# Kernel tuning notes

Measured on AMD Instinct MI355X. Metric: run time of the kernel, lower is better.

## Reference

```python
import jax, jax.numpy as jnp
jax.config.update("jax_enable_x64", True)
import numpy as np

B, S, D, H = 2, 1024, 1024, 16
DEPTH = D // H  # 64


def setup_inputs() -> dict:
    key = jax.random.key(0)
    ks = jax.random.split(key, 12)
    inp = {
        "q": jax.random.normal(ks[0], (B, S, D), jnp.float32),
        "k": jax.random.normal(ks[1], (B, S, D), jnp.float32),
        "v": jax.random.normal(ks[2], (B, S - 1, D), jnp.float32),
        "e": jnp.zeros((1,), jnp.float32),  # unused by the layer
        "mask": jax.random.randint(ks[3], (B, S - 1, S - 1), 0, 2, jnp.int32),
        "Wq": jax.random.normal(ks[4], (D, D), jnp.float32) * 0.02,
        "bq": jnp.zeros((D,), jnp.float32),
        "Wk": jax.random.normal(ks[5], (D, D), jnp.float32) * 0.02,
        "bk": jnp.zeros((D,), jnp.float32),
        "Wv": jax.random.normal(ks[6], (D, D), jnp.float32) * 0.02,
        "bv": jnp.zeros((D,), jnp.float32),
        "Wo": jax.random.normal(ks[7], (D, D), jnp.float32) * 0.02,
        "bo": jnp.zeros((D,), jnp.float32),
    }
    return inp


def _split_heads(x, b):
    # [b, s, D] -> [b, H, s, DEPTH]
    return x.reshape(b, -1, H, DEPTH).transpose(0, 2, 1, 3)


def reference(q, k, v, e, mask, Wq, bq, Wk, bk, Wv, bv, Wo, bo):
    b = q.shape[0]
    qh = _split_heads(q @ Wq + bq, b)  # [b,H,S,dh]
    kh = _split_heads(k @ Wk + bk, b)  # [b,H,S,dh]
    vh = _split_heads(v @ Wv + bv, b)  # [b,H,S-1,dh]
    # QK^T then asymmetric offset slice [1:, :-1]
    scores = jnp.einsum("bhqd,bhkd->bhqk", qh, kh)[:, :, 1:, :-1]  # [b,H,S-1,S-1]
    inv_sqrt_dk = 1.0 / jnp.sqrt(jnp.float32(DEPTH))
    nl_qk = jax.nn.relu(scores * inv_sqrt_dk).astype(jnp.float64)
    nl_qk = nl_qk + mask[:, None, :, :].astype(jnp.float64) * (-1e9)
    att_weights = jax.nn.softmax(nl_qk, axis=-1)  # fp64, [b,H,S-1,S-1]
    out = jnp.einsum("bhqk,bhkd->bhqd", att_weights, vh.astype(jnp.float64))
    out = out.transpose(0, 2, 1, 3).reshape(b, -1, H * DEPTH)  # [b,S-1,D]
    output = out.astype(jnp.float32) @ Wo + bo
    return (output, att_weights)
```

## Files before the change

kernel.cpp:

```cpp
#include <hip/hip_runtime.h>
#include <math.h>

#define HN 16
#define SEQ 1024
#define DMODEL 1024
#define DH 64
#define SM1 1023

typedef float  f32x4  __attribute__((ext_vector_type(4)));
typedef __bf16 bf16x8 __attribute__((ext_vector_type(8)));

#define GLD16(gsrc, ldst) \
    __builtin_amdgcn_global_load_lds((const __attribute__((address_space(1))) void*)(gsrc), \
                                     (__attribute__((address_space(3))) void*)(ldst), 16, 0, 0)

template<int MODE>
__global__ __launch_bounds__(256)
void gemm_mfma_kernel(const float* __restrict__ X, const float* __restrict__ W,
                      const float* __restrict__ bias, float* __restrict__ out32,
                      __bf16* __restrict__ outHi, __bf16* __restrict__ outLo,
                      int M, int rows)
{
    __shared__ __align__(16) __bf16 As[2][4096];
    __shared__ __align__(16) __bf16 Bs[2][4096];

    const int t  = threadIdx.x;
    const int w  = t >> 6, l = t & 63;
    const int lr = l & 15, ls = l >> 4;
    const int m0 = blockIdx.y * 64, n0 = blockIdx.x * 64;
    const int sr  = t >> 2;
    const int skq = t & 3;
    const bool arow_ok = (m0 + sr < M);

    f32x4 acc[4];
#pragma unroll
    for (int ct = 0; ct < 4; ++ct) acc[ct] = f32x4{0.f, 0.f, 0.f, 0.f};

    const int ar   = w * 16 + lr;
    const int a_hi = ar * 128 + (((2 * ls    ) ^ (ar & 7)) << 4);
    const int a_lo = ar * 128 + (((2 * ls + 1) ^ (ar & 7)) << 4);
    const int st_hi = sr * 128 + (((2 * skq    ) ^ (sr & 7)) << 4);
    const int st_lo = sr * 128 + (((2 * skq + 1) ^ (sr & 7)) << 4);

    float4 xv0, xv1;
    float  wv[8];

    auto LOADT = [&](int k0) {
        if (arow_ok) {
            xv0 = *(const float4*)&X[(size_t)(m0 + sr) * DMODEL + k0 + skq * 8];
            xv1 = *(const float4*)&X[(size_t)(m0 + sr) * DMODEL + k0 + skq * 8 + 4];
        } else {
            xv0 = float4{0.f, 0.f, 0.f, 0.f};
            xv1 = float4{0.f, 0.f, 0.f, 0.f};
        }
#pragma unroll
        for (int e = 0; e < 8; ++e)
            wv[e] = W[(size_t)(k0 + skq * 8 + e) * DMODEL + n0 + sr];
    };
    auto WRITET = [&](int buf) {
        float xa[8] = {xv0.x, xv0.y, xv0.z, xv0.w, xv1.x, xv1.y, xv1.z, xv1.w};
        bf16x8 ah8, al8, bh8, bl8;
#pragma unroll
        for (int e = 0; e < 8; ++e) {
            __bf16 hb = (__bf16)xa[e];
            ah8[e] = hb;
            al8[e] = (__bf16)(xa[e] - (float)hb);
            __bf16 wb = (__bf16)wv[e];
            bh8[e] = wb;
            bl8[e] = (__bf16)(wv[e] - (float)wb);
        }
        *(bf16x8*)((char*)As[buf] + st_hi) = ah8;
        *(bf16x8*)((char*)As[buf] + st_lo) = al8;
        *(bf16x8*)((char*)Bs[buf] + st_hi) = bh8;
        *(bf16x8*)((char*)Bs[buf] + st_lo) = bl8;
    };

    LOADT(0);
    WRITET(0);

    for (int ks = 0; ks < 32; ++ks) {
        const int cur = ks & 1;
        if (ks < 31) LOADT((ks + 1) * 32);
        __syncthreads();

        const bf16x8 ah = *(const bf16x8*)((const char*)As[cur] + a_hi);
        const bf16x8 al = *(const bf16x8*)((const char*)As[cur] + a_lo);
#pragma unroll
        for (int ct = 0; ct < 4; ++ct) {
            const int bc   = ct * 16 + lr;
            const int b_hi = bc * 128 + (((2 * ls    ) ^ (bc & 7)) << 4);
            const int b_lo = bc * 128 + (((2 * ls + 1) ^ (bc & 7)) << 4);
            const bf16x8 bh = *(const bf16x8*)((const char*)Bs[cur] + b_hi);
            const bf16x8 bl = *(const bf16x8*)((const char*)Bs[cur] + b_lo);
            acc[ct] = __builtin_amdgcn_mfma_f32_16x16x32_bf16(ah, bh, acc[ct], 0, 0, 0);
            acc[ct] = __builtin_amdgcn_mfma_f32_16x16x32_bf16(al, bh, acc[ct], 0, 0, 0);
            acc[ct] = __builtin_amdgcn_mfma_f32_16x16x32_bf16(ah, bl, acc[ct], 0, 0, 0);
        }
        if (ks < 31) WRITET(cur ^ 1);
    }

#pragma unroll
    for (int ct = 0; ct < 4; ++ct) {
        const int n = n0 + ct * 16 + lr;
        const float bv = bias[n];
#pragma unroll
        for (int j = 0; j < 4; ++j) {
            const int m = m0 + w * 16 + ls * 4 + j;
            if (m >= M) continue;
            const float val = acc[ct][j] + bv;
            if (MODE == 1) {
                out32[(size_t)m * DMODEL + n] = val;
            } else {
                const int bb = m / rows, s = m - bb * rows;
                const __bf16 hb = (__bf16)val;
                const __bf16 lb = (__bf16)(val - (float)hb);
                size_t idx;
                if (MODE == 0)
                    idx = (((size_t)(bb * HN + (n >> 6)) * SEQ + s) << 6) + (n & 63);
                else
                    idx = (((size_t)(bb * HN + (n >> 6)) * DH + (n & 63)) << 10) + s;
                outHi[idx] = hb; outLo[idx] = lb;
            }
        }
    }
}

__global__ __launch_bounds__(256)
void mask_pack_kernel(const int* __restrict__ mask, unsigned int* __restrict__ mb)
{
    const int row = blockIdx.x * 4 + (threadIdx.x >> 6);
    const int l   = threadIdx.x & 63;
    if (row >= 2 * SM1) return;
    const int* mrow = mask + (size_t)row * SM1;
    unsigned int* out = mb + (size_t)row * 32;
#pragma unroll
    for (int i = 0; i < 16; ++i) {
        const int c = i * 64 + l;
        const bool mv = (c < SM1) && (mrow[c] != 0);
        unsigned long long bal = __ballot(mv);
        if (l == 0) {
            out[i * 2]     = (unsigned int)bal;
            out[i * 2 + 1] = (unsigned int)(bal >> 32);
        }
    }
}

__global__ __launch_bounds__(512, 4)
void attn_fused_kernel(const __bf16* __restrict__ qhi, const __bf16* __restrict__ qlo,
                       const __bf16* __restrict__ khi, const __bf16* __restrict__ klo,
                       const __bf16* __restrict__ vthi, const __bf16* __restrict__ vtlo,
                       const unsigned int* __restrict__ mbG,
                       float* __restrict__ att, float* __restrict__ ctx)
{
    __shared__ __align__(16) char QE[17408];
    __shared__ __align__(16) char Kb[2][16384];
    __shared__ __align__(16) char Vb[16384];
    __shared__ unsigned int mbitsT[32][64];
    __shared__ float invs[64];
    __shared__ float partial[64][2];

    const int id  = blockIdx.x;
    const int xcd = id & 7, slot = id >> 3;
    const int bh  = xcd + 8 * (slot >> 4);
    const int b   = bh >> 4, h = bh & 15;
    const int q0  = (slot & 15) * 64;

    const int t = threadIdx.x, w = t >> 6, l = t & 63;
    const int lr = l & 15, ls = l >> 4;
    const int g = w & 3, p = w >> 2;

#define KDMA(c0_, b_) {                                                         \
    _Pragma("unroll")                                                           \
    for (int i_ = 0; i_ < 2; ++i_) {                                            \
        const int seg_ = w * 2 + i_;                                            \
        const int r_ = seg_ * 4 + (l >> 4);                                     \
        const int cw_ = (l & 15) ^ (r_ & 15);                                   \
        int krow_ = (c0_) + r_; if (krow_ > 1023) krow_ = 1023;                 \
        const __bf16* src_ = ((cw_ >> 3) ? klo : khi)                           \
            + ((size_t)bh * SEQ + krow_) * DH + (cw_ & 7) * 8;                  \
        GLD16(src_, Kb[b_] + seg_ * 1024);                                      \
    } }
#define VDMA(c0_) {                                                             \
    _Pragma("unroll")                                                           \
    for (int i_ = 0; i_ < 2; ++i_) {                                            \
        const int seg_ = w * 2 + i_;                                            \
        const int dr_ = seg_ * 4 + (l >> 4);                                    \
        const int cw_ = (l & 15) ^ (dr_ & 15);                                  \
        const __bf16* src_ = ((cw_ >> 3) ? vtlo : vthi)                         \
            + (((size_t)bh * DH + dr_) << 10) + (c0_) + (cw_ & 7) * 8;          \
        GLD16(src_, Vb + seg_ * 1024);                                          \
    } }

#pragma unroll
    for (int i = 0; i < 2; ++i) {
        const int seg = w * 2 + i;
        const int r = seg * 4 + (l >> 4);
        const int cw = (l & 15) ^ (r & 15);
        int qrow = q0 + r + 1; if (qrow > 1023) qrow = 1023;
        const __bf16* src = ((cw >> 3) ? qlo : qhi)
            + ((size_t)bh * SEQ + qrow) * DH + (cw & 7) * 8;
        GLD16(src, QE + seg * 1024);
    }
    KDMA(0, 0);
#pragma unroll
    for (int it = 0; it < 4; ++it) {
        const int idm = t + it * 512;
        const int cw = idm & 31, r = idm >> 5;
        const int rr = q0 + r;
        mbitsT[cw][r] = (rr < SM1) ? mbG[((size_t)b * SM1 + rr) * 32 + cw] : 0u;
    }
    __syncthreads();

    const int arow = g * 16 + lr;
    const bf16x8 a0h = *(const bf16x8*)(QE + arow * 256 + (((ls     ) ^ lr) << 4));
    const bf16x8 a1h = *(const bf16x8*)(QE + arow * 256 + ((( 4 + ls) ^ lr) << 4));
    const bf16x8 a0l = *(const bf16x8*)(QE + arow * 256 + ((( 8 + ls) ^ lr) << 4));
    const bf16x8 a1l = *(const bf16x8*)(QE + arow * 256 + (((12 + ls) ^ lr) << 4));
    __syncthreads();

    float rsum[4] = {0.f, 0.f, 0.f, 0.f};
    for (int kt = 0; kt < 16; ++kt) {
        const int c0 = kt * 64;
        const char* KB = Kb[kt & 1];
        if (kt < 15) KDMA(c0 + 64, (kt + 1) & 1);

#pragma unroll
        for (int i = 0; i < 2; ++i) {
            const int ct = p * 2 + i;
            const int kr16 = ct * 16 + lr;
            const bf16x8 b0h = *(const bf16x8*)(KB + kr16 * 256 + (((ls     ) ^ lr) << 4));
            const bf16x8 b1h = *(const bf16x8*)(KB + kr16 * 256 + ((( 4 + ls) ^ lr) << 4));
            const bf16x8 b0l = *(const bf16x8*)(KB + kr16 * 256 + ((( 8 + ls) ^ lr) << 4));
            const bf16x8 b1l = *(const bf16x8*)(KB + kr16 * 256 + (((12 + ls) ^ lr) << 4));

            f32x4 acc = {0.f, 0.f, 0.f, 0.f};
            __builtin_amdgcn_s_setprio(1);
            acc = __builtin_amdgcn_mfma_f32_16x16x32_bf16(a0h, b0h, acc, 0, 0, 0);
            acc = __builtin_amdgcn_mfma_f32_16x16x32_bf16(a0l, b0h, acc, 0, 0, 0);
            acc = __builtin_amdgcn_mfma_f32_16x16x32_bf16(a0h, b0l, acc, 0, 0, 0);
            acc = __builtin_amdgcn_mfma_f32_16x16x32_bf16(a1h, b1h, acc, 0, 0, 0);
            acc = __builtin_amdgcn_mfma_f32_16x16x32_bf16(a1l, b1h, acc, 0, 0, 0);
            acc = __builtin_amdgcn_mfma_f32_16x16x32_bf16(a1h, b1l, acc, 0, 0, 0);
            __builtin_amdgcn_s_setprio(0);

            const int c = c0 + ct * 16 + lr;
            const int wmi = kt * 2 + (ct >> 1);
#pragma unroll
            for (int j = 0; j < 4; ++j) {
                const int r = q0 + g * 16 + ls * 4 + j;
                if (r < SM1 && c < SM1) {
                    float sc = fmaxf(acc[j] * 0.125f, 0.f);
                    const unsigned int wm = mbitsT[wmi][g * 16 + ls * 4 + j];
                    if ((wm >> ((ct & 1) * 16 + lr)) & 1u) sc = -1e9f;
                    rsum[j] += __expf(sc);
                }
            }
        }
        __syncthreads();
    }

    KDMA(0, 0);

#pragma unroll
    for (int j = 0; j < 4; ++j) {
        rsum[j] += __shfl_xor(rsum[j], 1, 64);
        rsum[j] += __shfl_xor(rsum[j], 2, 64);
        rsum[j] += __shfl_xor(rsum[j], 4, 64);
        rsum[j] += __shfl_xor(rsum[j], 8, 64);
    }
    if (lr == 0) {
#pragma unroll
        for (int j = 0; j < 4; ++j)
            partial[g * 16 + ls * 4 + j][p] = rsum[j];
    }
    __syncthreads();
    if (t < 64) {
        const float s = partial[t][0] + partial[t][1];
        invs[t] = (q0 + t < SM1) ? 1.0f / s : 0.f;
    }
    __syncthreads();
    float inv4[4];
#pragma unroll
    for (int j = 0; j < 4; ++j) inv4[j] = invs[g * 16 + ls * 4 + j];

    float* E = (float*)QE;
    f32x4 oacc[4];
#pragma unroll
    for (int ct = 0; ct < 4; ++ct) oacc[ct] = f32x4{0.f, 0.f, 0.f, 0.f};

    for (int kt = 0; kt < 16; ++kt) {
        const int c0 = kt * 64;
        const char* KB = Kb[kt & 1];
        VDMA(c0);
        if (kt < 15) KDMA(c0 + 64, (kt + 1) & 1);

#pragma unroll
        for (int i = 0; i < 2; ++i) {
            const int ct = p * 2 + i;
            const int kr16 = ct * 16 + lr;
            const bf16x8 b0h = *(const bf16x8*)(KB + kr16 * 256 + (((ls     ) ^ lr) << 4));
            const bf16x8 b1h = *(const bf16x8*)(KB + kr16 * 256 + ((( 4 + ls) ^ lr) << 4));
            const bf16x8 b0l = *(const bf16x8*)(KB + kr16 * 256 + ((( 8 + ls) ^ lr) << 4));
            const bf16x8 b1l = *(const bf16x8*)(KB + kr16 * 256 + (((12 + ls) ^ lr) << 4));

            f32x4 acc = {0.f, 0.f, 0.f, 0.f};
            __builtin_amdgcn_s_setprio(1);
            acc = __builtin_amdgcn_mfma_f32_16x16x32_bf16(a0h, b0h, acc, 0, 0, 0);
            acc = __builtin_amdgcn_mfma_f32_16x16x32_bf16(a0l, b0h, acc, 0, 0, 0);
            acc = __builtin_amdgcn_mfma_f32_16x16x32_bf16(a0h, b0l, acc, 0, 0, 0);
            acc = __builtin_amdgcn_mfma_f32_16x16x32_bf16(a1h, b1h, acc, 0, 0, 0);
            acc = __builtin_amdgcn_mfma_f32_16x16x32_bf16(a1l, b1h, acc, 0, 0, 0);
            acc = __builtin_amdgcn_mfma_f32_16x16x32_bf16(a1h, b1l, acc, 0, 0, 0);
            __builtin_amdgcn_s_setprio(0);

            const int c = c0 + ct * 16 + lr;
            const int wmi = kt * 2 + (ct >> 1);
#pragma unroll
            for (int j = 0; j < 4; ++j) {
                const int r = q0 + g * 16 + ls * 4 + j;
                float v = 0.f;
                if (r < SM1 && c < SM1) {
                    float sc = fmaxf(acc[j] * 0.125f, 0.f);
                    const unsigned int wm = mbitsT[wmi][g * 16 + ls * 4 + j];
                    if ((wm >> ((ct & 1) * 16 + lr)) & 1u) sc = -1e9f;
                    v = __expf(sc) * inv4[j];
                }
                E[(g * 16 + ls * 4 + j) * 68 + ct * 16 + lr] = v;
            }
        }
        __syncthreads();

#pragma unroll
        for (int it = 0; it < 2; ++it) {
            const int idw = t + it * 512;
            const int r = idw >> 4, q4 = idw & 15;
            const int rr = q0 + r, cc = c0 + q4 * 4;
            if (rr < SM1) {
                f32x4 vv = *(const f32x4*)&E[r * 68 + q4 * 4];
                float* dst = &att[((size_t)bh * SM1 + rr) * SM1 + cc];
                if (cc + 4 <= SM1) {
                    __builtin_nontemporal_store(vv, (f32x4*)dst);
                } else {
                    if (cc + 0 < SM1) dst[0] = vv.x;
                    if (cc + 1 < SM1) dst[1] = vv.y;
                    if (cc + 2 < SM1) dst[2] = vv.z;
                }
            }
        }

        {
            const int pr = g * 16 + lr;
            const f32x4 p0 = *(const f32x4*)&E[pr * 68 + p * 32 + ls * 8];
            const f32x4 p1 = *(const f32x4*)&E[pr * 68 + p * 32 + ls * 8 + 4];
            float pf[8] = {p0.x, p0.y, p0.z, p0.w, p1.x, p1.y, p1.z, p1.w};
            bf16x8 ph, pl;
#pragma unroll
            for (int e = 0; e < 8; ++e) {
                const __bf16 hb = (__bf16)pf[e];
                ph[e] = hb;
                pl[e] = (__bf16)(pf[e] - (float)hb);
            }
#pragma unroll
            for (int ct = 0; ct < 4; ++ct) {
                const int vr16 = ct * 16 + lr;
                const bf16x8 vh = *(const bf16x8*)(Vb + vr16 * 256 + (((p * 4 + ls    ) ^ lr) << 4));
                const bf16x8 vl = *(const bf16x8*)(Vb + vr16 * 256 + (((8 + p * 4 + ls) ^ lr) << 4));
                __builtin_amdgcn_s_setprio(1);
                oacc[ct] = __builtin_amdgcn_mfma_f32_16x16x32_bf16(ph, vh, oacc[ct], 0, 0, 0);
                oacc[ct] = __builtin_amdgcn_mfma_f32_16x16x32_bf16(pl, vh, oacc[ct], 0, 0, 0);
                oacc[ct] = __builtin_amdgcn_mfma_f32_16x16x32_bf16(ph, vl, oacc[ct], 0, 0, 0);
                __builtin_amdgcn_s_setprio(0);
            }
        }
        __syncthreads();
    }

    float* red = (float*)QE;
    if (p == 1) {
#pragma unroll
        for (int ct = 0; ct < 4; ++ct)
#pragma unroll
            for (int j = 0; j < 4; ++j)
                red[(g * 16 + ls * 4 + j) * 68 + ct * 16 + lr] = oacc[ct][j];
    }
    __syncthreads();
    if (p == 0) {
#pragma unroll
        for (int ct = 0; ct < 4; ++ct)
#pragma unroll
            for (int j = 0; j < 4; ++j) {
                const int r = q0 + g * 16 + ls * 4 + j;
                if (r < SM1)
                    ctx[((size_t)b * SM1 + r) * DMODEL + h * DH + ct * 16 + lr] =
                        oacc[ct][j] + red[(g * 16 + ls * 4 + j) * 68 + ct * 16 + lr];
            }
    }
#undef KDMA
#undef VDMA
}

extern "C" void kernel_launch(void* const* d_in, const int* in_sizes, int n_in,
                              void* d_out, int out_size, void* d_ws, size_t ws_size,
                              hipStream_t stream) {
    const float* q    = (const float*)d_in[0];
    const float* k    = (const float*)d_in[1];
    const float* v    = (const float*)d_in[2];
    const int*   mask = (const int*)  d_in[4];
    const float* Wq   = (const float*)d_in[5];
    const float* bq   = (const float*)d_in[6];
    const float* Wk   = (const float*)d_in[7];
    const float* bk   = (const float*)d_in[8];
    const float* Wv   = (const float*)d_in[9];
    const float* bv   = (const float*)d_in[10];
    const float* Wo   = (const float*)d_in[11];
    const float* bo   = (const float*)d_in[12];

    float* out0 = (float*)d_out;
    float* att  = out0 + (size_t)2 * SM1 * DMODEL;

    const size_t NQ  = (size_t)2 * HN * SEQ * DH;
    const size_t NVT = (size_t)2 * HN * DH * 1024;
    __bf16* ws16 = (__bf16*)d_ws;
    __bf16* qhi  = ws16;
    __bf16* qlo  = qhi + NQ;
    __bf16* khi  = qlo + NQ;
    __bf16* klo  = khi + NQ;
    __bf16* vthi = klo + NQ;
    __bf16* vtlo = vthi + NVT;
    float*  ctx  = (float*)(vtlo + NVT);
    unsigned int* mbG = (unsigned int*)(ctx + (size_t)2 * SM1 * DMODEL);

    (void)hipMemsetAsync(vthi, 0, 2 * NVT * sizeof(__bf16), stream);

    mask_pack_kernel<<<dim3(512), 256, 0, stream>>>(mask, mbG);

    gemm_mfma_kernel<0><<<dim3(16, 32), 256, 0, stream>>>(q, Wq, bq, nullptr, qhi, qlo, 2 * SEQ, SEQ);
    gemm_mfma_kernel<0><<<dim3(16, 32), 256, 0, stream>>>(k, Wk, bk, nullptr, khi, klo, 2 * SEQ, SEQ);
    gemm_mfma_kernel<2><<<dim3(16, 32), 256, 0, stream>>>(v, Wv, bv, nullptr, vthi, vtlo, 2 * SM1, SM1);

    attn_fused_kernel<<<dim3(512), 512, 0, stream>>>(qhi, qlo, khi, klo, vthi, vtlo, mbG, att, ctx);

    gemm_mfma_kernel<1><<<dim3(16, 32), 256, 0, stream>>>(ctx, Wo, bo, out0, nullptr, nullptr, 2 * SM1, SM1);
}
```

Baseline: 244.6 us.

## Pre-split inputs and weights to bf16 hi/lo, stage GEMM tiles via LDS DMA

```diff
diff --git a/kernel.cpp b/kernel.cpp
--- a/kernel.cpp
+++ b/kernel.cpp
@@ -14,23 +14,72 @@
     __builtin_amdgcn_global_load_lds((const __attribute__((address_space(1))) void*)(gsrc), \
                                      (__attribute__((address_space(3))) void*)(ldst), 16, 0, 0)
 
+__global__ __launch_bounds__(256)
+void split_kernel(const float* __restrict__ src, __bf16* __restrict__ hi,
+                  __bf16* __restrict__ lo, int nchunks)
+{
+    for (int i = blockIdx.x * 256 + threadIdx.x; i < nchunks; i += gridDim.x * 256) {
+        float4 v0 = *(const float4*)&src[(size_t)i * 8];
+        float4 v1 = *(const float4*)&src[(size_t)i * 8 + 4];
+        float xa[8] = {v0.x, v0.y, v0.z, v0.w, v1.x, v1.y, v1.z, v1.w};
+        bf16x8 h8, l8;
+#pragma unroll
+        for (int e = 0; e < 8; ++e) {
+            __bf16 hb = (__bf16)xa[e];
+            h8[e] = hb;
+            l8[e] = (__bf16)(xa[e] - (float)hb);
+        }
+        *(bf16x8*)&hi[(size_t)i * 8] = h8;
+        *(bf16x8*)&lo[(size_t)i * 8] = l8;
+    }
+}
+
+__global__ __launch_bounds__(256)
+void splitT_kernel(const float* __restrict__ W, __bf16* __restrict__ thi,
+                   __bf16* __restrict__ tlo)
+{
+    __shared__ float T[64][65];
+    const int t = threadIdx.x;
+    const int r0 = blockIdx.y * 64, c0 = blockIdx.x * 64;
+#pragma unroll
+    for (int it = 0; it < 4; ++it) {
+        const int rl = (t >> 4) + it * 16;
+        const int cl = (t & 15) * 4;
+        float4 v = *(const float4*)&W[(size_t)(r0 + rl) * 1024 + c0 + cl];
+        T[cl + 0][rl] = v.x; T[cl + 1][rl] = v.y;
+        T[cl + 2][rl] = v.z; T[cl + 3][rl] = v.w;
+    }
+    __syncthreads();
+    const int nl = t >> 2, ch = t & 3;
+    float vals[16];
+#pragma unroll
+    for (int e = 0; e < 16; ++e) vals[e] = T[nl][ch * 16 + e];
+    bf16x8 h0, h1, l0, l1;
+#pragma unroll
+    for (int e = 0; e < 8; ++e) {
+        __bf16 hb = (__bf16)vals[e];
+        h0[e] = hb; l0[e] = (__bf16)(vals[e] - (float)hb);
+        __bf16 hb2 = (__bf16)vals[8 + e];
+        h1[e] = hb2; l1[e] = (__bf16)(vals[8 + e] - (float)hb2);
+    }
+    const size_t base = (size_t)(c0 + nl) * 1024 + r0 + ch * 16;
+    *(bf16x8*)&thi[base] = h0; *(bf16x8*)&thi[base + 8] = h1;
+    *(bf16x8*)&tlo[base] = l0; *(bf16x8*)&tlo[base + 8] = l1;
+}
+
 template<int MODE>
 __global__ __launch_bounds__(256)
-void gemm_mfma_kernel(const float* __restrict__ X, const float* __restrict__ W,
+void gemm_bf16_kernel(const __bf16* __restrict__ Ahi, const __bf16* __restrict__ Alo,
+                      const __bf16* __restrict__ Bhi, const __bf16* __restrict__ Blo,
                       const float* __restrict__ bias, float* __restrict__ out32,
                       __bf16* __restrict__ outHi, __bf16* __restrict__ outLo,
                       int M, int rows)
 {
-    __shared__ __align__(16) __bf16 As[2][4096];
-    __shared__ __align__(16) __bf16 Bs[2][4096];
-
-    const int t  = threadIdx.x;
-    const int w  = t >> 6, l = t & 63;
+    __shared__ __align__(16) char LB[32768];
+
+    const int t = threadIdx.x, w = t >> 6, l = t & 63;
     const int lr = l & 15, ls = l >> 4;
     const int m0 = blockIdx.y * 64, n0 = blockIdx.x * 64;
-    const int sr  = t >> 2;
-    const int skq = t & 3;
-    const bool arow_ok = (m0 + sr < M);
 
     f32x4 acc[4];
 #pragma unroll
@@ -39,87 +88,111 @@
     const int ar   = w * 16 + lr;
     const int a_hi = ar * 128 + (((2 * ls    ) ^ (ar & 7)) << 4);
     const int a_lo = ar * 128 + (((2 * ls + 1) ^ (ar & 7)) << 4);
-    const int st_hi = sr * 128 + (((2 * skq    ) ^ (sr & 7)) << 4);
-    const int st_lo = sr * 128 + (((2 * skq + 1) ^ (sr & 7)) << 4);
-
-    float4 xv0, xv1;
-    float  wv[8];
-
-    auto LOADT = [&](int k0) {
-        if (arow_ok) {
-            xv0 = *(const float4*)&X[(size_t)(m0 + sr) * DMODEL + k0 + skq * 8];
-            xv1 = *(const float4*)&X[(size_t)(m0 + sr) * DMODEL + k0 + skq * 8 + 4];
-        } else {
-            xv0 = float4{0.f, 0.f, 0.f, 0.f};
-            xv1 = float4{0.f, 0.f, 0.f, 0.f};
-        }
-#pragma unroll
-        for (int e = 0; e < 8; ++e)
-            wv[e] = W[(size_t)(k0 + skq * 8 + e) * DMODEL + n0 + sr];
-    };
-    auto WRITET = [&](int buf) {
-        float xa[8] = {xv0.x, xv0.y, xv0.z, xv0.w, xv1.x, xv1.y, xv1.z, xv1.w};
-        bf16x8 ah8, al8, bh8, bl8;
-#pragma unroll
-        for (int e = 0; e < 8; ++e) {
-            __bf16 hb = (__bf16)xa[e];
-            ah8[e] = hb;
-            al8[e] = (__bf16)(xa[e] - (float)hb);
-            __bf16 wb = (__bf16)wv[e];
-            bh8[e] = wb;
-            bl8[e] = (__bf16)(wv[e] - (float)wb);
-        }
-        *(bf16x8*)((char*)As[buf] + st_hi) = ah8;
-        *(bf16x8*)((char*)As[buf] + st_lo) = al8;
-        *(bf16x8*)((char*)Bs[buf] + st_hi) = bh8;
-        *(bf16x8*)((char*)Bs[buf] + st_lo) = bl8;
-    };
-
-    LOADT(0);
-    WRITET(0);
+
+#define GSTAGE(k0_, buf_) {                                                       \
+    _Pragma("unroll")                                                             \
+    for (int i_ = 0; i_ < 2; ++i_) {                                              \
+        const int r_  = (w * 2 + i_) * 8 + (l >> 3);                              \
+        const int un_ = (l & 7) ^ (r_ & 7);                                       \
+        const __bf16* sa_ = ((un_ & 1) ? Alo : Ahi)                               \
+            + (size_t)(m0 + r_) * 1024 + (k0_) + (un_ >> 1) * 8;                  \
+        GLD16(sa_, LB + (buf_) * 8192 + (w * 2 + i_) * 1024);                     \
+        const __bf16* sb_ = ((un_ & 1) ? Blo : Bhi)                               \
+            + (size_t)(n0 + r_) * 1024 + (k0_) + (un_ >> 1) * 8;                  \
+        GLD16(sb_, LB + 16384 + (buf_) * 8192 + (w * 2 + i_) * 1024);             \
+    } }
+
+    GSTAGE(0, 0);
+    __syncthreads();
 
     for (int ks = 0; ks < 32; ++ks) {
         const int cur = ks & 1;
-        if (ks < 31) LOADT((ks + 1) * 32);
-        __syncthreads();
-
-        const bf16x8 ah = *(const bf16x8*)((const char*)As[cur] + a_hi);
-        const bf16x8 al = *(const bf16x8*)((const char*)As[cur] + a_lo);
+        if (ks < 31) GSTAGE((ks + 1) * 32, cur ^ 1);
+
+        const char* As = LB + cur * 8192;
+        const char* Bs = LB + 16384 + cur * 8192;
+        const bf16x8 ah = *(const bf16x8*)(As + a_hi);
+        const bf16x8 al = *(const bf16x8*)(As + a_lo);
+        __builtin_amdgcn_s_setprio(1);
 #pragma unroll
         for (int ct = 0; ct < 4; ++ct) {
             const int bc   = ct * 16 + lr;
             const int b_hi = bc * 128 + (((2 * ls    ) ^ (bc & 7)) << 4);
             const int b_lo = bc * 128 + (((2 * ls + 1) ^ (bc & 7)) << 4);
-            const bf16x8 bh = *(const bf16x8*)((const char*)Bs[cur] + b_hi);
-            const bf16x8 bl = *(const bf16x8*)((const char*)Bs[cur] + b_lo);
+            const bf16x8 bh = *(const bf16x8*)(Bs + b_hi);
+            const bf16x8 bl = *(const bf16x8*)(Bs + b_lo);
             acc[ct] = __builtin_amdgcn_mfma_f32_16x16x32_bf16(ah, bh, acc[ct], 0, 0, 0);
             acc[ct] = __builtin_amdgcn_mfma_f32_16x16x32_bf16(al, bh, acc[ct], 0, 0, 0);
             acc[ct] = __builtin_amdgcn_mfma_f32_16x16x32_bf16(ah, bl, acc[ct], 0, 0, 0);
         }
-        if (ks < 31) WRITET(cur ^ 1);
-    }
-
-#pragma unroll
-    for (int ct = 0; ct < 4; ++ct) {
-        const int n = n0 + ct * 16 + lr;
-        const float bv = bias[n];
-#pragma unroll
-        for (int j = 0; j < 4; ++j) {
-            const int m = m0 + w * 16 + ls * 4 + j;
-            if (m >= M) continue;
-            const float val = acc[ct][j] + bv;
-            if (MODE == 1) {
-                out32[(size_t)m * DMODEL + n] = val;
-            } else {
-                const int bb = m / rows, s = m - bb * rows;
-                const __bf16 hb = (__bf16)val;
-                const __bf16 lb = (__bf16)(val - (float)hb);
-                size_t idx;
-                if (MODE == 0)
-                    idx = (((size_t)(bb * HN + (n >> 6)) * SEQ + s) << 6) + (n & 63);
-                else
-                    idx = (((size_t)(bb * HN + (n >> 6)) * DH + (n & 63)) << 10) + s;
-                outHi[idx] = hb; outLo[idx] = lb;
+        __builtin_amdgcn_s_setprio(0);
+        __syncthreads();
+    }
+#undef GSTAGE
+
+    if (MODE == 2) {
+        float* T = (float*)LB;
+#pragma unroll
+        for (int ct = 0; ct < 4; ++ct) {
+            const int nl = ct * 16 + lr;
+            const float bv = bias[n0 + nl];
+#pragma unroll
+            for (int j = 0; j < 4; ++j)
+                T[nl * 65 + w * 16 + ls * 4 + j] = acc[ct][j] + bv;
+        }
+        __syncthreads();
+        const int dr = t >> 2, ch = t & 3;
+        const int hh = n0 >> 6;
+        const int mb = m0 + ch * 16;
+        float vals[16];
+#pragma unroll
+        for (int e = 0; e < 16; ++e) vals[e] = T[dr * 65 + ch * 16 + e];
+        const int bb0 = mb / rows;
+        const int s0  = mb - bb0 * rows;
+        if (mb + 15 < M && bb0 == (mb + 15) / rows && (s0 & 7) == 0) {
+            bf16x8 h0, h1, l0, l1;
+#pragma unroll
+            for (int e = 0; e < 8; ++e) {
+                __bf16 hb = (__bf16)vals[e];
+                h0[e] = hb; l0[e] = (__bf16)(vals[e] - (float)hb);
+                __bf16 hb2 = (__bf16)vals[8 + e];
+                h1[e] = hb2; l1[e] = (__bf16)(vals[8 + e] - (float)hb2);
+            }
+            const size_t base = (((size_t)(bb0 * HN + hh) * DH + dr) << 10) + s0;
+            *(bf16x8*)&outHi[base] = h0; *(bf16x8*)&outHi[base + 8] = h1;
+            *(bf16x8*)&outLo[base] = l0; *(bf16x8*)&outLo[base + 8] = l1;
+        } else {
+#pragma unroll
+            for (int e = 0; e < 16; ++e) {
+                const int m = mb + e;
+                if (m < M) {
+                    const int bb = m / rows, s = m - bb * rows;
+                    const size_t idx = (((size_t)(bb * HN + hh) * DH + dr) << 10) + s;
+                    const __bf16 hb = (__bf16)vals[e];
+                    outHi[idx] = hb;
+                    outLo[idx] = (__bf16)(vals[e] - (float)hb);
+                }
+            }
+        }
+    } else {
+#pragma unroll
+        for (int ct = 0; ct < 4; ++ct) {
+            const int n = n0 + ct * 16 + lr;
+            const float bv = bias[n];
+#pragma unroll
+            for (int j = 0; j < 4; ++j) {
+                const int m = m0 + w * 16 + ls * 4 + j;
+                if (m >= M) continue;
+                const float val = acc[ct][j] + bv;
+                if (MODE == 1) {
+                    out32[(size_t)m * DMODEL + n] = val;
+                } else {
+                    const int bb = m / rows, s = m - bb * rows;
+                    const __bf16 hb = (__bf16)val;
+                    const __bf16 lb = (__bf16)(val - (float)hb);
+                    const size_t idx = (((size_t)(bb * HN + (n >> 6)) * SEQ + s) << 6) + (n & 63);
+                    outHi[idx] = hb; outLo[idx] = lb;
+                }
             }
         }
     }
@@ -150,7 +223,8 @@
                        const __bf16* __restrict__ khi, const __bf16* __restrict__ klo,
                        const __bf16* __restrict__ vthi, const __bf16* __restrict__ vtlo,
                        const unsigned int* __restrict__ mbG,
-                       float* __restrict__ att, float* __restrict__ ctx)
+                       float* __restrict__ att,
+                       __bf16* __restrict__ ctxHi, __bf16* __restrict__ ctxLo)
 {
     __shared__ __align__(16) char QE[17408];
     __shared__ __align__(16) char Kb[2][16384];
@@ -390,9 +464,15 @@
 #pragma unroll
             for (int j = 0; j < 4; ++j) {
                 const int r = q0 + g * 16 + ls * 4 + j;
-                if (r < SM1)
-                    ctx[((size_t)b * SM1 + r) * DMODEL + h * DH + ct * 16 + lr] =
+                if (r < SM1) {
+                    const float val =
                         oacc[ct][j] + red[(g * 16 + ls * 4 + j) * 68 + ct * 16 + lr];
+                    const size_t idx =
+                        ((size_t)b * SM1 + r) * DMODEL + h * DH + ct * 16 + lr;
+                    const __bf16 hb = (__bf16)val;
+                    ctxHi[idx] = hb;
+                    ctxLo[idx] = (__bf16)(val - (float)hb);
+                }
             }
     }
 #undef KDMA
@@ -418,27 +498,49 @@
     float* out0 = (float*)d_out;
     float* att  = out0 + (size_t)2 * SM1 * DMODEL;
 
-    const size_t NQ  = (size_t)2 * HN * SEQ * DH;
+    const size_t NX  = (size_t)2048 * 1024;
+    const size_t NW  = (size_t)1024 * 1024;
+    const size_t NQH = (size_t)2 * HN * SEQ * DH;
     const size_t NVT = (size_t)2 * HN * DH * 1024;
-    __bf16* ws16 = (__bf16*)d_ws;
-    __bf16* qhi  = ws16;
-    __bf16* qlo  = qhi + NQ;
-    __bf16* khi  = qlo + NQ;
-    __bf16* klo  = khi + NQ;
-    __bf16* vthi = klo + NQ;
-    __bf16* vtlo = vthi + NVT;
-    float*  ctx  = (float*)(vtlo + NVT);
-    unsigned int* mbG = (unsigned int*)(ctx + (size_t)2 * SM1 * DMODEL);
-
-    (void)hipMemsetAsync(vthi, 0, 2 * NVT * sizeof(__bf16), stream);
+
+    __bf16* p2  = (__bf16*)d_ws;
+    __bf16* qSh = p2; p2 += NX;  __bf16* qSl = p2; p2 += NX;
+    __bf16* kSh = p2; p2 += NX;  __bf16* kSl = p2; p2 += NX;
+    __bf16* vSh = p2; p2 += NX;  __bf16* vSl = p2; p2 += NX;
+    __bf16* WqTh = p2; p2 += NW; __bf16* WqTl = p2; p2 += NW;
+    __bf16* WkTh = p2; p2 += NW; __bf16* WkTl = p2; p2 += NW;
+    __bf16* WvTh = p2; p2 += NW; __bf16* WvTl = p2; p2 += NW;
+    __bf16* WoTh = p2; p2 += NW; __bf16* WoTl = p2; p2 += NW;
+    __bf16* qhh = p2; p2 += NQH; __bf16* qhl = p2; p2 += NQH;
+    __bf16* khh = p2; p2 += NQH; __bf16* khl = p2; p2 += NQH;
+    __bf16* vth = p2; p2 += NVT; __bf16* vtl = p2; p2 += NVT;
+    unsigned int* mbG = (unsigned int*)p2;
+    __bf16* ctxHi = qSh;
+    __bf16* ctxLo = qSl;
+
+    (void)hipMemsetAsync(vth, 0, 2 * NVT * sizeof(__bf16), stream);
 
     mask_pack_kernel<<<dim3(512), 256, 0, stream>>>(mask, mbG);
 
-    gemm_mfma_kernel<0><<<dim3(16, 32), 256, 0, stream>>>(q, Wq, bq, nullptr, qhi, qlo, 2 * SEQ, SEQ);
-    gemm_mfma_kernel<0><<<dim3(16, 32), 256, 0, stream>>>(k, Wk, bk, nullptr, khi, klo, 2 * SEQ, SEQ);
-    gemm_mfma_kernel<2><<<dim3(16, 32), 256, 0, stream>>>(v, Wv, bv, nullptr, vthi, vtlo, 2 * SM1, SM1);
-
-    attn_fused_kernel<<<dim3(512), 512, 0, stream>>>(qhi, qlo, khi, klo, vthi, vtlo, mbG, att, ctx);
-
-    gemm_mfma_kernel<1><<<dim3(16, 32), 256, 0, stream>>>(ctx, Wo, bo, out0, nullptr, nullptr, 2 * SM1, SM1);
+    split_kernel<<<dim3(1024), 256, 0, stream>>>(q, qSh, qSl, 2048 * 1024 / 8);
+    split_kernel<<<dim3(1024), 256, 0, stream>>>(k, kSh, kSl, 2048 * 1024 / 8);
+    split_kernel<<<dim3(1024), 256, 0, stream>>>(v, vSh, vSl, 2046 * 1024 / 8);
+
+    splitT_kernel<<<dim3(16, 16), 256, 0, stream>>>(Wq, WqTh, WqTl);
+    splitT_kernel<<<dim3(16, 16), 256, 0, stream>>>(Wk, WkTh, WkTl);
+    splitT_kernel<<<dim3(16, 16), 256, 0, stream>>>(Wv, WvTh, WvTl);
+    splitT_kernel<<<dim3(16, 16), 256, 0, stream>>>(Wo, WoTh, WoTl);
+
+    gemm_bf16_kernel<0><<<dim3(16, 32), 256, 0, stream>>>(qSh, qSl, WqTh, WqTl, bq,
+                                                          nullptr, qhh, qhl, 2 * SEQ, SEQ);
+    gemm_bf16_kernel<0><<<dim3(16, 32), 256, 0, stream>>>(kSh, kSl, WkTh, WkTl, bk,
+                                                          nullptr, khh, khl, 2 * SEQ, SEQ);
+    gemm_bf16_kernel<2><<<dim3(16, 32), 256, 0, stream>>>(vSh, vSl, WvTh, WvTl, bv,
+                                                          nullptr, vth, vtl, 2 * SM1, SM1);
+
+    attn_fused_kernel<<<dim3(512), 512, 0, stream>>>(qhh, qhl, khh, khl, vth, vtl,
+                                                     mbG, att, ctxHi, ctxLo);
+
+    gemm_bf16_kernel<1><<<dim3(16, 32), 256, 0, stream>>>(ctxHi, ctxLo, WoTh, WoTl, bo,
+                                                          out0, nullptr, nullptr, 2 * SM1, SM1);
 }
```

Result: faster. 239.6 us (-2.0%).
